# Performance work log

Hardware: AMD Instinct MI355X
Metric: run time of the kernel (lower is better)

## Reference

```python
import jax, jax.numpy as jnp
import numpy as np

EPS = 1e-12  # torch F.normalize default eps


def setup_inputs() -> dict:
    key = jax.random.key(0)
    ks = jax.random.split(key, 4)
    b, c, h, w = 2, 192, 256, 256
    num_heads = 4
    x = jax.random.normal(ks[0], (b, c, h, w), dtype=jnp.float32)
    w_qkv = jax.random.normal(ks[1], (3 * c, c), dtype=jnp.float32) * 0.02
    w_dw = jax.random.normal(ks[2], (3 * c, 1, 3, 3), dtype=jnp.float32) * 0.1
    w_proj = jax.random.normal(ks[3], (c, c), dtype=jnp.float32) * 0.02
    temperature = jnp.ones((num_heads, 1, 1), dtype=jnp.float32)
    return {"x": x, "w_qkv": w_qkv, "w_dw": w_dw, "w_proj": w_proj,
            "temperature": temperature, "num_heads": num_heads}


def reference(x, w_qkv, w_dw, w_proj, temperature, num_heads):
    b, c, h, w = x.shape
    ch = c // num_heads
    # 1x1 conv (pointwise GEMM) then depthwise 3x3 conv
    qkv = jnp.einsum('bchw,oc->bohw', x, w_qkv)
    qkv = jax.lax.conv_general_dilated(
        qkv, w_dw, window_strides=(1, 1), padding='SAME',
        dimension_numbers=('NCHW', 'OIHW', 'NCHW'),
        feature_group_count=3 * c)
    q, k, v = jnp.split(qkv, 3, axis=1)
    # b (head c) h w -> b head (c h) w
    def to_heads(t):
        return t.reshape(b, num_heads, ch * h, w)
    q, k, v = to_heads(q), to_heads(k), to_heads(v)
    # L2-normalize over the (c h) axis
    def l2n(t):
        n = jnp.sqrt(jnp.sum(t * t, axis=-2, keepdims=True))
        return t / jnp.maximum(n, EPS)
    q, k = l2n(q), l2n(k)
    # channel-transposed attention over width: attn is (b, head, w, w)
    attn = jnp.einsum('bhcw,bhcv->bhwv', q, k) * temperature[None]
    attn = jax.nn.softmax(attn, axis=-2)  # softmax over dim=-2 as in source
    out = jnp.einsum('bhcw,bhwv->bhcv', v, attn)
    out = out.reshape(b, c, h, w)
    return jnp.einsum('bchw,oc->bohw', out, w_proj)
```

## Files before the change

kernel.cpp:

```cpp
#include <hip/hip_runtime.h>
#include <math.h>

#define HW 65536

typedef float f32x4 __attribute__((ext_vector_type(4)));
typedef short bf16x8 __attribute__((ext_vector_type(8)));
typedef short bf16x4 __attribute__((ext_vector_type(4)));

static constexpr size_t OFF_A0    = 0;
static constexpr size_t OFF_SP    = 100663296;
static constexpr size_t OFF_QKT   = 150994944;
static constexpr size_t OFF_VPL   = 251658240;
static constexpr size_t OFF_PT    = 301989888;
static constexpr size_t OFF_NORMS = 303038464;
static constexpr size_t OFF_WQ    = 303054848;
static constexpr size_t OFF_WP    = 303276032;

__device__ inline float b2f(unsigned short u) { union { unsigned u; float f; } v; v.u = ((unsigned)u) << 16; return v.f; }
__device__ inline unsigned short f2b(float f) {
    union { float f; unsigned u; } v; v.f = f;
    return (unsigned short)((v.u + 0x7fffu + ((v.u >> 16) & 1u)) >> 16);
}

__global__ __launch_bounds__(256) void conv_w(const float* __restrict__ wq, const float* __restrict__ wp,
                                              unsigned short* __restrict__ wqb, unsigned short* __restrict__ wpb)
{
    int t = blockIdx.x * 256 + threadIdx.x;
    int stride = gridDim.x * 256;
    for (int i = t; i < 576 * 192; i += stride) wqb[i] = f2b(wq[i]);
    for (int i = t; i < 192 * 192; i += stride) wpb[i] = f2b(wp[i]);
}

template <int MODE>
__global__ __launch_bounds__(256) void gemm_pm3(const unsigned short* __restrict__ Aw,
                                                const void* __restrict__ Bsrc,
                                                unsigned short* __restrict__ outb,
                                                float* __restrict__ outf, int Mtiles)
{
    __shared__ unsigned short Bs[192 * 130];
    int tid = threadIdx.x;
    int w = tid >> 6, lane = tid & 63, lg = lane >> 4, li = lane & 15;
    int wm = w >> 1, wn = w & 1;
    const int b = (int)(blockIdx.x >> 9);
    const long px0 = (long)(blockIdx.x & 511) * 128;

    if (MODE == 0) {
        const float* X = (const float*)Bsrc;
#pragma unroll
        for (int it = 0; it < 24; ++it) {
            int task = it * 256 + tid;
            int ch = task >> 5, seg = task & 31;
            float4 v = *(const float4*)(X + ((long)(b * 192 + ch)) * HW + px0 + seg * 4);
            unsigned* d32 = (unsigned*)&Bs[ch * 130 + seg * 4];
            d32[0] = (unsigned)f2b(v.x) | ((unsigned)f2b(v.y) << 16);
            d32[1] = (unsigned)f2b(v.z) | ((unsigned)f2b(v.w) << 16);
        }
    } else {
        const unsigned short* X = (const unsigned short*)Bsrc;
#pragma unroll
        for (int it = 0; it < 12; ++it) {
            int task = it * 256 + tid;
            int ch = task >> 4, seg = task & 15;
            bf16x8 v = *(const bf16x8*)(X + ((long)(b * 192 + ch)) * HW + px0 + seg * 8);
            unsigned* d32 = (unsigned*)&Bs[ch * 130 + seg * 8];
            const unsigned* s32 = (const unsigned*)&v;
            d32[0] = s32[0]; d32[1] = s32[1]; d32[2] = s32[2]; d32[3] = s32[3];
        }
    }
    __syncthreads();

    bf16x8 Bf[4][6];
#pragma unroll
    for (int fb = 0; fb < 4; ++fb) {
        int px = wn * 64 + fb * 16 + li;
#pragma unroll
        for (int ks = 0; ks < 6; ++ks) {
            bf16x8 v;
#pragma unroll
            for (int e = 0; e < 8; ++e)
                v[e] = (short)Bs[(ks * 32 + lg * 8 + e) * 130 + px];
            Bf[fb][ks] = v;
        }
    }

    const int pxl = (int)(px0) + wn * 64;
    const int Mtot = Mtiles * 64;

    for (int mt = 0; mt < Mtiles; ++mt) {
        int oc0 = mt * 64;
        const unsigned short* ab = Aw + (long)(oc0 + wm * 32 + li) * 192 + lg * 8;
        f32x4 acc[2][4];
#pragma unroll
        for (int i = 0; i < 2; ++i)
#pragma unroll
            for (int j = 0; j < 4; ++j) acc[i][j] = (f32x4){0.f, 0.f, 0.f, 0.f};
#pragma unroll
        for (int ks = 0; ks < 6; ++ks) {
            bf16x8 a0 = *(const bf16x8*)(ab + ks * 32);
            bf16x8 a1 = *(const bf16x8*)(ab + 16 * 192 + ks * 32);
#pragma unroll
            for (int fb = 0; fb < 4; ++fb) {
                acc[0][fb] = __builtin_amdgcn_mfma_f32_16x16x32_bf16(a0, Bf[fb][ks], acc[0][fb], 0, 0, 0);
                acc[1][fb] = __builtin_amdgcn_mfma_f32_16x16x32_bf16(a1, Bf[fb][ks], acc[1][fb], 0, 0, 0);
            }
        }
#pragma unroll
        for (int fa = 0; fa < 2; ++fa) {
            int m = oc0 + wm * 32 + fa * 16 + lg * 4;
#pragma unroll
            for (int fb = 0; fb < 4; ++fb) {
                int px = pxl + fb * 16 + li;
                long base = ((long)b * Mtot + m) * HW + px;
#pragma unroll
                for (int ii = 0; ii < 4; ++ii) {
                    if (MODE == 1) outf[base + (long)ii * HW] = acc[fa][fb][ii];
                    else           outb[base + (long)ii * HW] = f2b(acc[fa][fb][ii]);
                }
            }
        }
    }
}

__global__ __launch_bounds__(256) void dwconv2(const unsigned short* __restrict__ in,
                                               const float* __restrict__ wdw,
                                               unsigned short* __restrict__ qkT,
                                               unsigned short* __restrict__ vpl)
{
    __shared__ unsigned short Ls[34 * 272];
    int tid = threadIdx.x;
    int zp = blockIdx.y;
    int b = zp / 576, ch3 = zp % 576;
    int y0 = blockIdx.x * 32;
    const unsigned short* ip = in + (long)zp * HW;
    float w9[9];
#pragma unroll
    for (int t = 0; t < 9; ++t) w9[t] = wdw[ch3 * 9 + t];

    const bf16x8 z8 = (bf16x8){0, 0, 0, 0, 0, 0, 0, 0};
    if (tid < 34)               *(bf16x8*)&Ls[tid * 272] = z8;
    else if (tid < 68)          *(bf16x8*)&Ls[(tid - 34) * 272 + 264] = z8;
#pragma unroll
    for (int it = 0; it < 5; ++it) {
        int task = it * 256 + tid;
        if (task < 1088) {
            int r = task >> 5, seg = task & 31;
            int gy = y0 - 1 + r;
            bf16x8 v = z8;
            if (gy >= 0 && gy < 256) v = *(const bf16x8*)(ip + gy * 256 + seg * 8);
            *(bf16x8*)&Ls[r * 272 + 8 + seg * 8] = v;
        }
    }
    __syncthreads();

    int xg = tid & 63, yg = tid >> 6;
    int x0 = xg * 4;
    float acc[8][4];
#pragma unroll
    for (int yy = 0; yy < 8; ++yy)
#pragma unroll
        for (int xi = 0; xi < 4; ++xi) acc[yy][xi] = 0.f;

#pragma unroll
    for (int rr = 0; rr < 10; ++rr) {
        const unsigned short* lp = &Ls[(yg * 8 + rr) * 272 + 8 + x0];
        bf16x4 A  = *(const bf16x4*)(lp - 4);
        bf16x4 Bv = *(const bf16x4*)(lp);
        bf16x4 Cv = *(const bf16x4*)(lp + 4);
        float f[6] = { b2f((unsigned short)A[3]),  b2f((unsigned short)Bv[0]),
                       b2f((unsigned short)Bv[1]), b2f((unsigned short)Bv[2]),
                       b2f((unsigned short)Bv[3]), b2f((unsigned short)Cv[0]) };
#pragma unroll
        for (int dy = 0; dy < 3; ++dy) {
            int yy = rr - dy;
            if (yy >= 0 && yy < 8) {
#pragma unroll
                for (int dx = 0; dx < 3; ++dx)
#pragma unroll
                    for (int xi = 0; xi < 4; ++xi)
                        acc[yy][xi] = fmaf(w9[dy * 3 + dx], f[dx + xi], acc[yy][xi]);
            }
        }
    }

    if (ch3 < 384) {
        int isk = ch3 >= 192 ? 1 : 0;
        int chq = ch3 - isk * 192;
        int hh = chq / 48, cc = chq % 48;
        long zbase = (long)(b * 8 + isk * 4 + hh) * 3145728L + (long)cc * 256 + y0 + yg * 8;
#pragma unroll
        for (int xi = 0; xi < 4; ++xi) {
            bf16x8 pv;
#pragma unroll
            for (int yy = 0; yy < 8; ++yy) pv[yy] = (short)f2b(acc[yy][xi]);
            *(bf16x8*)(qkT + zbase + (long)(x0 + xi) * 12288) = pv;
        }
    } else {
        unsigned short* ob = vpl + (long)(b * 192 + ch3 - 384) * HW + (long)(y0 + yg * 8) * 256 + x0;
#pragma unroll
        for (int yy = 0; yy < 8; ++yy) {
            bf16x4 pv;
#pragma unroll
            for (int xi = 0; xi < 4; ++xi) pv[xi] = (short)f2b(acc[yy][xi]);
            *(bf16x4*)(ob + yy * 256) = pv;
        }
    }
}

__global__ __launch_bounds__(256) void norms_k(const unsigned short* __restrict__ qkT, float* __restrict__ norms)
{
    int i = blockIdx.x, z = blockIdx.y;
    const unsigned short* p = qkT + ((long)z * 256 + i) * 12288 + threadIdx.x * 8;
    float s = 0.f;
#pragma unroll
    for (int it = 0; it < 6; ++it) {
        bf16x8 v = *(const bf16x8*)(p + it * 2048);
#pragma unroll
        for (int e = 0; e < 8; ++e) { float f = b2f((unsigned short)v[e]); s = fmaf(f, f, s); }
    }
    for (int off = 32; off > 0; off >>= 1) s += __shfl_down(s, off, 64);
    __shared__ float r4[4];
    if ((threadIdx.x & 63) == 0) r4[threadIdx.x >> 6] = s;
    __syncthreads();
    if (threadIdx.x == 0) {
        float t = r4[0] + r4[1] + r4[2] + r4[3];
        norms[z * 256 + i] = 1.0f / fmaxf(sqrtf(t), 1e-12f);
    }
}

__global__ __launch_bounds__(256) void attn_qk(const unsigned short* __restrict__ qkT, float* __restrict__ Sp)
{
    __shared__ unsigned short Qs[128 * 40];
    __shared__ unsigned short Ks[128 * 40];
    int tid = threadIdx.x;
    int z = blockIdx.z; int bh = z >> 4, sk = z & 15; int b = bh >> 2, h = bh & 3;
    const unsigned short* qT = qkT + (long)(b * 8 + h) * 3145728;
    const unsigned short* kT = qkT + (long)(b * 8 + 4 + h) * 3145728;
    int i0 = blockIdx.x * 128, j0 = blockIdx.y * 128;
    int w = tid >> 6, lane = tid & 63, lg = lane >> 4, li = lane & 15;
    int wm = w >> 1, wn = w & 1;
    int srow = tid >> 2, sseg = (tid & 3) * 8;
    long qoff = (long)(i0 + srow) * 12288 + sk * 768 + sseg;
    long koff = (long)(j0 + srow) * 12288 + sk * 768 + sseg;

    f32x4 acc[4][4];
#pragma unroll
    for (int i = 0; i < 4; ++i)
#pragma unroll
        for (int j = 0; j < 4; ++j) acc[i][j] = (f32x4){0.f, 0.f, 0.f, 0.f};

    bf16x8 qr0 = *(const bf16x8*)(qT + qoff);
    bf16x8 qr1 = *(const bf16x8*)(qT + qoff + (long)64 * 12288);
    bf16x8 kr0 = *(const bf16x8*)(kT + koff);
    bf16x8 kr1 = *(const bf16x8*)(kT + koff + (long)64 * 12288);

#pragma unroll 1
    for (int ks = 0; ks < 24; ++ks) {
        *(bf16x8*)&Qs[srow * 40 + sseg] = qr0;
        *(bf16x8*)&Qs[(64 + srow) * 40 + sseg] = qr1;
        *(bf16x8*)&Ks[srow * 40 + sseg] = kr0;
        *(bf16x8*)&Ks[(64 + srow) * 40 + sseg] = kr1;
        if (ks < 23) {
            long o = (long)(ks + 1) * 32;
            qr0 = *(const bf16x8*)(qT + qoff + o);
            qr1 = *(const bf16x8*)(qT + qoff + (long)64 * 12288 + o);
            kr0 = *(const bf16x8*)(kT + koff + o);
            kr1 = *(const bf16x8*)(kT + koff + (long)64 * 12288 + o);
        }
        __syncthreads();
        bf16x8 af[4], bfr[4];
#pragma unroll
        for (int fa = 0; fa < 4; ++fa)
            af[fa] = *(const bf16x8*)&Qs[(wm * 64 + fa * 16 + li) * 40 + lg * 8];
#pragma unroll
        for (int fb = 0; fb < 4; ++fb)
            bfr[fb] = *(const bf16x8*)&Ks[(wn * 64 + fb * 16 + li) * 40 + lg * 8];
#pragma unroll
        for (int fa = 0; fa < 4; ++fa)
#pragma unroll
            for (int fb = 0; fb < 4; ++fb)
                acc[fa][fb] = __builtin_amdgcn_mfma_f32_16x16x32_bf16(af[fa], bfr[fb], acc[fa][fb], 0, 0, 0);
        __syncthreads();
    }

    float* op = Sp + ((long)(sk * 8 + bh) << 16);
#pragma unroll
    for (int fa = 0; fa < 4; ++fa) {
        int i = i0 + wm * 64 + fa * 16 + lg * 4;
#pragma unroll
        for (int fb = 0; fb < 4; ++fb) {
            int j = j0 + wn * 64 + fb * 16 + li;
#pragma unroll
            for (int ii = 0; ii < 4; ++ii)
                op[(long)(i + ii) * 256 + j] = acc[fa][fb][ii];
        }
    }
}

__global__ __launch_bounds__(256) void softmax_k(const float* __restrict__ Sp, const float* __restrict__ norms,
                                                 const float* __restrict__ temp, unsigned short* __restrict__ Pt)
{
    __shared__ float Sd[256 * 9];
    __shared__ float red[32 * 9];
    int tid = threadIdx.x;
    int g = blockIdx.x; int bh = g >> 5, jq = g & 31; int b = bh >> 2, h = bh & 3;
    int jl = tid & 7, iq = tid >> 3;
    int j = jq * 8 + jl;
    const float* nq = norms + (b * 8 + h) * 256;
    float invkj = norms[(b * 8 + 4 + h) * 256 + j] * temp[h];
    const float* sp = Sp + (long)bh * HW + j;

    float m = -1e30f;
#pragma unroll
    for (int ii = 0; ii < 8; ++ii) {
        int i = iq * 8 + ii;
        float s = 0.f;
#pragma unroll
        for (int sk = 0; sk < 16; ++sk) s += sp[((long)(sk * 8) << 16) + i * 256];
        float v = s * nq[i] * invkj;
        Sd[i * 9 + jl] = v;
        m = fmaxf(m, v);
    }
    red[iq * 9 + jl] = m;
    __syncthreads();
    m = -1e30f;
#pragma unroll
    for (int s2 = 0; s2 < 32; ++s2) m = fmaxf(m, red[s2 * 9 + jl]);
    __syncthreads();
    float sum = 0.f;
#pragma unroll
    for (int ii = 0; ii < 8; ++ii) sum += __expf(Sd[(iq * 8 + ii) * 9 + jl] - m);
    red[iq * 9 + jl] = sum;
    __syncthreads();
    sum = 0.f;
#pragma unroll
    for (int s2 = 0; s2 < 32; ++s2) sum += red[s2 * 9 + jl];
    float rs = 1.0f / sum;

    int fb = jq >> 1, li2 = (jq & 1) * 8 + jl;
    int ks = iq >> 2, lg = iq & 3;
    unsigned short* pt = Pt + (long)bh * HW + (long)((fb * 8 + ks) * 64 + lg * 16 + li2) * 8;
    bf16x8 pv;
#pragma unroll
    for (int ii = 0; ii < 8; ++ii)
        pv[ii] = (short)f2b(__expf(Sd[(iq * 8 + ii) * 9 + jl] - m) * rs);
    *(bf16x8*)pt = pv;
}

__global__ __launch_bounds__(256) void vattn(const unsigned short* __restrict__ vpl,
                                             const unsigned short* __restrict__ Pt,
                                             unsigned short* __restrict__ vout)
{
    int tid = threadIdx.x;
    int w = tid >> 6, lane = tid & 63, lg = lane >> 4, li = lane & 15;
    int wm = w >> 1, wn = w & 1;
    int m0 = blockIdx.x * 64 + wm * 32;
    int bh = blockIdx.y; int b = bh >> 2, h = bh & 3;
    const unsigned short* V = vpl + (long)(b * 192 + h * 48) * HW;
    const unsigned short* P = Pt + (long)bh * HW + wn * 32768 + lane * 8;

    f32x4 acc[2][8];
#pragma unroll
    for (int i = 0; i < 2; ++i)
#pragma unroll
        for (int j = 0; j < 8; ++j) acc[i][j] = (f32x4){0.f, 0.f, 0.f, 0.f};

#pragma unroll 2
    for (int ks = 0; ks < 8; ++ks) {
        bf16x8 a0 = *(const bf16x8*)(V + (long)(m0 + li) * 256 + ks * 32 + lg * 8);
        bf16x8 a1 = *(const bf16x8*)(V + (long)(m0 + 16 + li) * 256 + ks * 32 + lg * 8);
#pragma unroll
        for (int fb2 = 0; fb2 < 8; ++fb2) {
            bf16x8 bb = *(const bf16x8*)(P + (fb2 * 8 + ks) * 512);
            acc[0][fb2] = __builtin_amdgcn_mfma_f32_16x16x32_bf16(a0, bb, acc[0][fb2], 0, 0, 0);
            acc[1][fb2] = __builtin_amdgcn_mfma_f32_16x16x32_bf16(a1, bb, acc[1][fb2], 0, 0, 0);
        }
    }
    unsigned short* ob = vout + (long)(b * 192 + h * 48) * HW;
#pragma unroll
    for (int fa = 0; fa < 2; ++fa) {
#pragma unroll
        for (int fb2 = 0; fb2 < 8; ++fb2) {
            int j = (wn * 8 + fb2) * 16 + li;
#pragma unroll
            for (int ii = 0; ii < 4; ++ii) {
                int m = m0 + fa * 16 + lg * 4 + ii;
                ob[((long)(m >> 8) << 16) + ((m & 255) << 8) + j] = f2b(acc[fa][fb2][ii]);
            }
        }
    }
}

extern "C" void kernel_launch(void* const* d_in, const int* in_sizes, int n_in,
                              void* d_out, int out_size, void* d_ws, size_t ws_size,
                              hipStream_t stream)
{
    (void)in_sizes; (void)n_in; (void)out_size; (void)ws_size;
    const float* x      = (const float*)d_in[0];
    const float* w_qkv  = (const float*)d_in[1];
    const float* w_dw   = (const float*)d_in[2];
    const float* w_proj = (const float*)d_in[3];
    const float* temp   = (const float*)d_in[4];
    float* out = (float*)d_out;
    char* ws = (char*)d_ws;

    unsigned short* qkv_pre = (unsigned short*)(ws + OFF_A0);
    float*          Sp      = (float*)(ws + OFF_SP);
    unsigned short* vout    = (unsigned short*)(ws + OFF_A0);
    unsigned short* qkT     = (unsigned short*)(ws + OFF_QKT);
    unsigned short* vpl     = (unsigned short*)(ws + OFF_VPL);
    unsigned short* Pt      = (unsigned short*)(ws + OFF_PT);
    float*          norms   = (float*)(ws + OFF_NORMS);
    unsigned short* wqb     = (unsigned short*)(ws + OFF_WQ);
    unsigned short* wpb     = (unsigned short*)(ws + OFF_WP);

    conv_w<<<64, 256, 0, stream>>>(w_qkv, w_proj, wqb, wpb);
    gemm_pm3<0><<<1024, 256, 0, stream>>>(wqb, (const void*)x, qkv_pre, nullptr, 9);
    dwconv2<<<dim3(8, 1152), 256, 0, stream>>>(qkv_pre, w_dw, qkT, vpl);
    norms_k<<<dim3(256, 16), 256, 0, stream>>>(qkT, norms);
    attn_qk<<<dim3(2, 2, 128), 256, 0, stream>>>(qkT, Sp);
    softmax_k<<<256, 256, 0, stream>>>(Sp, norms, temp, Pt);
    vattn<<<dim3(192, 8), 256, 0, stream>>>(vpl, Pt, vout);
    gemm_pm3<1><<<1024, 256, 0, stream>>>(wpb, (const void*)vout, nullptr, out, 3);
}
```

Baseline: 317.3 us.

## Use LDS transpose reads with blocked layout and halve pointwise GEMM pixel tile

The pointwise GEMM kernels now stage the activation tile in LDS in a 4-channel by 16-pixel blocked layout. They load B fragments with ds_read_b64_tr_b16 transpose reads instead of 48 scalar strided LDS reads per fragment set. The pixel tile per block shrinks from 128 to 64 and the grid doubles, which lowers register pressure and raises parallelism. The cost is that each block re-reads the weight matrix for only half as many pixels.

```diff
diff --git a/kernel.cpp b/kernel.cpp
--- a/kernel.cpp
+++ b/kernel.cpp
@@ -32,83 +32,98 @@
 }
 
 template <int MODE>
-__global__ __launch_bounds__(256) void gemm_pm3(const unsigned short* __restrict__ Aw,
+__global__ __launch_bounds__(256) void gemm_pm4(const unsigned short* __restrict__ Aw,
                                                 const void* __restrict__ Bsrc,
                                                 unsigned short* __restrict__ outb,
                                                 float* __restrict__ outf, int Mtiles)
 {
-    __shared__ unsigned short Bs[192 * 130];
+    __shared__ __align__(1024) unsigned short Bs[12288];
     int tid = threadIdx.x;
     int w = tid >> 6, lane = tid & 63, lg = lane >> 4, li = lane & 15;
     int wm = w >> 1, wn = w & 1;
-    const int b = (int)(blockIdx.x >> 9);
-    const long px0 = (long)(blockIdx.x & 511) * 128;
+    const int b = (int)(blockIdx.x >> 10);
+    const long px0 = (long)(blockIdx.x & 1023) * 64;
 
     if (MODE == 0) {
         const float* X = (const float*)Bsrc;
 #pragma unroll
-        for (int it = 0; it < 24; ++it) {
-            int task = it * 256 + tid;
-            int ch = task >> 5, seg = task & 31;
-            float4 v = *(const float4*)(X + ((long)(b * 192 + ch)) * HW + px0 + seg * 4);
-            unsigned* d32 = (unsigned*)&Bs[ch * 130 + seg * 4];
-            d32[0] = (unsigned)f2b(v.x) | ((unsigned)f2b(v.y) << 16);
-            d32[1] = (unsigned)f2b(v.z) | ((unsigned)f2b(v.w) << 16);
+        for (int it = 0; it < 12; ++it) {
+            int t = it * 256 + tid;
+            int ch  = (t & 3) + 4 * ((t >> 5) % 48);
+            int pxq = ((t >> 2) & 7) + 8 * ((t >> 5) / 48);
+            float4 v = *(const float4*)(X + ((long)(b * 192 + ch)) * HW + px0 + pxq * 4);
+            bf16x4 pv;
+            pv[0] = (short)f2b(v.x); pv[1] = (short)f2b(v.y);
+            pv[2] = (short)f2b(v.z); pv[3] = (short)f2b(v.w);
+            int px = pxq * 4;
+            *(bf16x4*)&Bs[(ch >> 2) * 256 + (px >> 4) * 64 + (ch & 3) * 16 + (px & 15)] = pv;
         }
     } else {
         const unsigned short* X = (const unsigned short*)Bsrc;
 #pragma unroll
-        for (int it = 0; it < 12; ++it) {
-            int task = it * 256 + tid;
-            int ch = task >> 4, seg = task & 15;
-            bf16x8 v = *(const bf16x8*)(X + ((long)(b * 192 + ch)) * HW + px0 + seg * 8);
-            unsigned* d32 = (unsigned*)&Bs[ch * 130 + seg * 8];
-            const unsigned* s32 = (const unsigned*)&v;
-            d32[0] = s32[0]; d32[1] = s32[1]; d32[2] = s32[2]; d32[3] = s32[3];
-        }
-    }
-    __syncthreads();
-
-    bf16x8 Bf[4][6];
-#pragma unroll
-    for (int fb = 0; fb < 4; ++fb) {
-        int px = wn * 64 + fb * 16 + li;
-#pragma unroll
-        for (int ks = 0; ks < 6; ++ks) {
-            bf16x8 v;
-#pragma unroll
-            for (int e = 0; e < 8; ++e)
-                v[e] = (short)Bs[(ks * 32 + lg * 8 + e) * 130 + px];
-            Bf[fb][ks] = v;
-        }
-    }
-
-    const int pxl = (int)(px0) + wn * 64;
+        for (int it = 0; it < 6; ++it) {
+            int t = it * 256 + tid;
+            int ch  = (t & 3) + 4 * ((t >> 4) % 48);
+            int pxo = ((t >> 2) & 3) + 4 * ((t >> 4) / 48);
+            bf16x8 v = *(const bf16x8*)(X + ((long)(b * 192 + ch)) * HW + px0 + pxo * 8);
+            int px = pxo * 8;
+            *(bf16x8*)&Bs[(ch >> 2) * 256 + (px >> 4) * 64 + (ch & 3) * 16 + (px & 15)] = v;
+        }
+    }
+    __syncthreads();
+
+    unsigned vb = (unsigned)(size_t)&Bs[(lane & 15) * 4 + (lane >> 4) * 512 + wn * 128];
+    bf16x4 tr[2][6][2];
+#define TRR(FB,KS,G,OFF) asm volatile("ds_read_b64_tr_b16 %0, %1 offset:" OFF \
+        : "=v"(tr[FB][KS][G]) : "v"(vb))
+    TRR(0,0,0,"0");     TRR(0,0,1,"512");
+    TRR(0,1,0,"4096");  TRR(0,1,1,"4608");
+    TRR(0,2,0,"8192");  TRR(0,2,1,"8704");
+    TRR(0,3,0,"12288"); TRR(0,3,1,"12800");
+    TRR(0,4,0,"16384"); TRR(0,4,1,"16896");
+    TRR(0,5,0,"20480"); TRR(0,5,1,"20992");
+    TRR(1,0,0,"128");   TRR(1,0,1,"640");
+    TRR(1,1,0,"4224");  TRR(1,1,1,"4736");
+    TRR(1,2,0,"8320");  TRR(1,2,1,"8832");
+    TRR(1,3,0,"12416"); TRR(1,3,1,"12928");
+    TRR(1,4,0,"16512"); TRR(1,4,1,"17024");
+    TRR(1,5,0,"20608"); TRR(1,5,1,"21120");
+#undef TRR
+    asm volatile("s_waitcnt lgkmcnt(0)" ::: "memory");
+    __builtin_amdgcn_sched_barrier(0);
+
+    bf16x8 Bf[2][6];
+#pragma unroll
+    for (int fb = 0; fb < 2; ++fb)
+#pragma unroll
+        for (int ks = 0; ks < 6; ++ks)
+            Bf[fb][ks] = __builtin_shufflevector(tr[fb][ks][0], tr[fb][ks][1], 0, 1, 2, 3, 4, 5, 6, 7);
+
+    const int pxl = (int)px0 + wn * 32;
     const int Mtot = Mtiles * 64;
 
     for (int mt = 0; mt < Mtiles; ++mt) {
         int oc0 = mt * 64;
         const unsigned short* ab = Aw + (long)(oc0 + wm * 32 + li) * 192 + lg * 8;
-        f32x4 acc[2][4];
+        f32x4 acc[2][2];
 #pragma unroll
         for (int i = 0; i < 2; ++i)
 #pragma unroll
-            for (int j = 0; j < 4; ++j) acc[i][j] = (f32x4){0.f, 0.f, 0.f, 0.f};
+            for (int j = 0; j < 2; ++j) acc[i][j] = (f32x4){0.f, 0.f, 0.f, 0.f};
 #pragma unroll
         for (int ks = 0; ks < 6; ++ks) {
             bf16x8 a0 = *(const bf16x8*)(ab + ks * 32);
             bf16x8 a1 = *(const bf16x8*)(ab + 16 * 192 + ks * 32);
-#pragma unroll
-            for (int fb = 0; fb < 4; ++fb) {
-                acc[0][fb] = __builtin_amdgcn_mfma_f32_16x16x32_bf16(a0, Bf[fb][ks], acc[0][fb], 0, 0, 0);
-                acc[1][fb] = __builtin_amdgcn_mfma_f32_16x16x32_bf16(a1, Bf[fb][ks], acc[1][fb], 0, 0, 0);
-            }
+            acc[0][0] = __builtin_amdgcn_mfma_f32_16x16x32_bf16(a0, Bf[0][ks], acc[0][0], 0, 0, 0);
+            acc[0][1] = __builtin_amdgcn_mfma_f32_16x16x32_bf16(a0, Bf[1][ks], acc[0][1], 0, 0, 0);
+            acc[1][0] = __builtin_amdgcn_mfma_f32_16x16x32_bf16(a1, Bf[0][ks], acc[1][0], 0, 0, 0);
+            acc[1][1] = __builtin_amdgcn_mfma_f32_16x16x32_bf16(a1, Bf[1][ks], acc[1][1], 0, 0, 0);
         }
 #pragma unroll
         for (int fa = 0; fa < 2; ++fa) {
             int m = oc0 + wm * 32 + fa * 16 + lg * 4;
 #pragma unroll
-            for (int fb = 0; fb < 4; ++fb) {
+            for (int fb = 0; fb < 2; ++fb) {
                 int px = pxl + fb * 16 + li;
                 long base = ((long)b * Mtot + m) * HW + px;
 #pragma unroll
@@ -414,11 +429,11 @@
     unsigned short* wpb     = (unsigned short*)(ws + OFF_WP);
 
     conv_w<<<64, 256, 0, stream>>>(w_qkv, w_proj, wqb, wpb);
-    gemm_pm3<0><<<1024, 256, 0, stream>>>(wqb, (const void*)x, qkv_pre, nullptr, 9);
+    gemm_pm4<0><<<2048, 256, 0, stream>>>(wqb, (const void*)x, qkv_pre, nullptr, 9);
     dwconv2<<<dim3(8, 1152), 256, 0, stream>>>(qkv_pre, w_dw, qkT, vpl);
     norms_k<<<dim3(256, 16), 256, 0, stream>>>(qkT, norms);
     attn_qk<<<dim3(2, 2, 128), 256, 0, stream>>>(qkT, Sp);
     softmax_k<<<256, 256, 0, stream>>>(Sp, norms, temp, Pt);
     vattn<<<dim3(192, 8), 256, 0, stream>>>(vpl, Pt, vout);
-    gemm_pm3<1><<<1024, 256, 0, stream>>>(wpb, (const void*)vout, nullptr, out, 3);
-}
+    gemm_pm4<1><<<2048, 256, 0, stream>>>(wpb, (const void*)vout, nullptr, out, 3);
+}
```

After: 379.3 us. +19.5%, slower.
